# Kernel tuning notes

Hardware: AMD Instinct MI355X
Metric: run time of the kernel (lower is better)

Reference implementation:

```python
import jax, jax.numpy as jnp
import numpy as np

EMB = 768
B, LD, LW, LH = 2, 8, 8, 8        # LR grid = number of windows per axis
HD, HW, HH = 32, 32, 32           # HR volume
LN_EPS = 1e-5


def setup_inputs() -> dict:
    key = jax.random.key(0)
    ks = jax.random.split(key, 12)
    s = 1.0 / np.sqrt(EMB)
    inp = {
        "LR_image": jax.random.normal(ks[0], (B, LD, LW, LH, EMB), jnp.float32),
        "HR_image": jax.random.normal(ks[1], (B, HD, HW, HH, EMB), jnp.float32),
        "Wq_w": jax.random.uniform(ks[2], (EMB, EMB), jnp.float32, -s, s),
        "Wq_b": jax.random.uniform(ks[3], (EMB,), jnp.float32, -s, s),
        "Wk_w": jax.random.uniform(ks[4], (EMB, EMB), jnp.float32, -s, s),
        "Wk_b": jax.random.uniform(ks[5], (EMB,), jnp.float32, -s, s),
        "Wv_w": jax.random.uniform(ks[6], (EMB, EMB), jnp.float32, -s, s),
        "Wv_b": jax.random.uniform(ks[7], (EMB,), jnp.float32, -s, s),
        "Wo_w": jax.random.uniform(ks[8], (EMB, EMB), jnp.float32, -s, s),
        "Wo_b": jax.random.uniform(ks[9], (EMB,), jnp.float32, -s, s),
        "ln_g": jnp.ones((EMB,), jnp.float32),
        "ln_b": jnp.zeros((EMB,), jnp.float32),
        "S_d": 4, "S_w": 4, "S_h": 4,
    }
    return inp


def _window_partition(x, S_d, S_w, S_h):
    # x: [B, D, W, H, C] -> [B, N_blocks, S_d*S_w*S_h, C]
    b, d, w, h, c = x.shape
    x = x.reshape(b, d // S_d, S_d, w // S_w, S_w, h // S_h, S_h, c)
    x = jnp.transpose(x, (0, 2, 4, 6, 1, 3, 5, 7))  # [B,Sd,Sw,Sh,Db,Wb,Hb,C]
    x = x.reshape(b, S_d * S_w * S_h, -1, c)
    return jnp.transpose(x, (0, 2, 1, 3))  # [B, N_blocks, S, C]


def reference(LR_image, HR_image, Wq_w, Wq_b, Wk_w, Wk_b, Wv_w, Wv_b,
              Wo_w, Wo_b, ln_g, ln_b, S_d, S_w, S_h):
    b = LR_image.shape[0]
    c = LR_image.shape[-1]
    # queries: [B, N, 1, C]
    q_in = LR_image.reshape(b, -1, c)[:, :, None, :]
    # windowed keys/values: [B, N, S, C]
    hr = _window_partition(HR_image, S_d, S_w, S_h)
    q = q_in @ Wq_w.T + Wq_b
    k = hr @ Wk_w.T + Wk_b
    v = hr @ Wv_w.T + Wv_b
    scale = 1.0 / jnp.sqrt(jnp.asarray(c, q.dtype))
    scores = jnp.einsum('bnqc,bnsc->bnqs', q, k) * scale  # [B,N,1,S]
    attn = jax.nn.softmax(scores, axis=-1)
    x = jnp.einsum('bnqs,bnsc->bnqc', attn, v).reshape(b, -1, c)
    x = x @ Wo_w.T + Wo_b
    res = q.reshape(b, -1, c) + x  # residual with projected queries
    mu = jnp.mean(res, axis=-1, keepdims=True)
    var = jnp.var(res, axis=-1, keepdims=True)
    return (res - mu) / jnp.sqrt(var + LN_EPS) * ln_g + ln_b
```

## Files before the change

### kernel.cpp

```cpp
#include <hip/hip_runtime.h>
#include <hip/hip_bf16.h>
#include <math.h>

#define EMB 768
#define NB 2
#define NWIN 512
#define NROWS (NB*NWIN)
#define SWIN 64
#define HRDIM 32
#define ROWF (NROWS*EMB)
#define WELEM (EMB*EMB)

using bfrag = __attribute__((ext_vector_type(8))) short;
using f32x4 = __attribute__((ext_vector_type(4))) float;

#define GL16(g, l)  __builtin_amdgcn_global_load_lds(                         \
    (const __attribute__((address_space(1))) void*)(g),                       \
    (__attribute__((address_space(3))) void*)(l), 16, 0, 0)

__global__ __launch_bounds__(256)
void f2b_kernel(const float* __restrict__ in, __hip_bfloat16* __restrict__ out,
                int n8) {
  int i = blockIdx.x * 256 + threadIdx.x;
  if (i >= n8) return;
  float4 a = *(const float4*)&in[(size_t)i * 8];
  float4 b = *(const float4*)&in[(size_t)i * 8 + 4];
  __hip_bfloat16 t[8];
  t[0] = __float2bfloat16(a.x); t[1] = __float2bfloat16(a.y);
  t[2] = __float2bfloat16(a.z); t[3] = __float2bfloat16(a.w);
  t[4] = __float2bfloat16(b.x); t[5] = __float2bfloat16(b.y);
  t[6] = __float2bfloat16(b.z); t[7] = __float2bfloat16(b.w);
  *(uint4*)&out[(size_t)i * 8] = *(const uint4*)t;
}

__global__ __launch_bounds__(256)
void f2b3_kernel(const float* __restrict__ inA, __hip_bfloat16* __restrict__ outA,
                 const float* __restrict__ inB, __hip_bfloat16* __restrict__ outB,
                 const float* __restrict__ inC, __hip_bfloat16* __restrict__ outC) {
  const float* in = (blockIdx.y == 0) ? inA : (blockIdx.y == 1) ? inB : inC;
  __hip_bfloat16* out = (blockIdx.y == 0) ? outA : (blockIdx.y == 1) ? outB : outC;
  int i = blockIdx.x * 256 + threadIdx.x;
  float4 a = *(const float4*)&in[(size_t)i * 8];
  float4 b = *(const float4*)&in[(size_t)i * 8 + 4];
  __hip_bfloat16 t[8];
  t[0] = __float2bfloat16(a.x); t[1] = __float2bfloat16(a.y);
  t[2] = __float2bfloat16(a.z); t[3] = __float2bfloat16(a.w);
  t[4] = __float2bfloat16(b.x); t[5] = __float2bfloat16(b.y);
  t[6] = __float2bfloat16(b.z); t[7] = __float2bfloat16(b.w);
  *(uint4*)&out[(size_t)i * 8] = *(const uint4*)t;
}

__global__ __launch_bounds__(256)
void f2bT_kernel(const float* __restrict__ in, __hip_bfloat16* __restrict__ out) {
  __shared__ float tile[32][33];
  const int bi = blockIdx.x, bj = blockIdx.y;
  const int c = threadIdx.x & 31, r8 = threadIdx.x >> 5;
#pragma unroll
  for (int rr = 0; rr < 4; ++rr) {
    int r = r8 + rr * 8;
    tile[c][r] = in[(size_t)(bi * 32 + r) * EMB + bj * 32 + c];
  }
  __syncthreads();
#pragma unroll
  for (int rr = 0; rr < 4; ++rr) {
    int n = r8 + rr * 8;
    out[(size_t)(bj * 32 + n) * EMB + bi * 32 + c] = __float2bfloat16(tile[n][c]);
  }
}

template<bool BIAS, bool WF32, bool WB16>
__global__ __launch_bounds__(256)
void gemm_bf16(const __hip_bfloat16* __restrict__ A,
               const __hip_bfloat16* __restrict__ Bm,
               const float* __restrict__ bias,
               float* __restrict__ Cf, __hip_bfloat16* __restrict__ Cb,
               int M, int N) {
  constexpr int K = EMB;
  constexpr int NT = K / 64;
  __shared__ short lsA[3][64 * 64];
  __shared__ short lsB[3][64 * 64];
  const int t = threadIdx.x;
  const int w = t >> 6, lane = t & 63;
  const int lr = lane & 15, lk = lane >> 4;
  const int m0 = blockIdx.y * 64, n0 = blockIdx.x * 64;

  const int r0 = t >> 3, c0 = t & 7;
  const int kc = c0 ^ (r0 & 7);
  const __hip_bfloat16* aptr0 = A + (size_t)(m0 + r0) * K + kc * 8;
  const __hip_bfloat16* aptr1 = A + (size_t)(m0 + r0 + 32) * K + kc * 8;
  const __hip_bfloat16* bptr0 = Bm + (size_t)(n0 + r0) * K + kc * 8;
  const __hip_bfloat16* bptr1 = Bm + (size_t)(n0 + r0 + 32) * K + kc * 8;
  const int wbase = w * 512;

  const int arow = w * 16 + lr;
  int aoff[2], boff[4][2];
#pragma unroll
  for (int ks = 0; ks < 2; ++ks)
    aoff[ks] = arow * 64 + (((ks << 2) | lk) ^ (arow & 7)) * 8;
#pragma unroll
  for (int f = 0; f < 4; ++f) {
    int br = f * 16 + lr;
#pragma unroll
    for (int ks = 0; ks < 2; ++ks)
      boff[f][ks] = br * 64 + (((ks << 2) | lk) ^ (br & 7)) * 8;
  }

  f32x4 acc[4];
#pragma unroll
  for (int f = 0; f < 4; ++f) acc[f] = (f32x4){0.f, 0.f, 0.f, 0.f};

#pragma unroll
  for (int p = 0; p < 2; ++p) {
    int ko = p * 64;
    GL16(aptr0 + ko, &lsA[p][wbase]);
    GL16(aptr1 + ko, &lsA[p][wbase + 2048]);
    GL16(bptr0 + ko, &lsB[p][wbase]);
    GL16(bptr1 + ko, &lsB[p][wbase + 2048]);
  }

#pragma unroll
  for (int kt = 0; kt < NT; ++kt) {
    if (kt + 2 < NT) {
      constexpr int s3[NT + 2] = {0,1,2,0,1,2,0,1,2,0,1,2,0,1};
      const int sl = s3[kt + 2];
      int ko = (kt + 2) * 64;
      GL16(aptr0 + ko, &lsA[sl][wbase]);
      GL16(aptr1 + ko, &lsA[sl][wbase + 2048]);
      GL16(bptr0 + ko, &lsB[sl][wbase]);
      GL16(bptr1 + ko, &lsB[sl][wbase + 2048]);
    }
    if (kt + 2 < NT)      asm volatile("s_waitcnt vmcnt(8)" ::: "memory");
    else if (kt + 1 < NT) asm volatile("s_waitcnt vmcnt(4)" ::: "memory");
    else                  asm volatile("s_waitcnt vmcnt(0)" ::: "memory");
    __builtin_amdgcn_sched_barrier(0);
    __builtin_amdgcn_s_barrier();

    const int cur = kt % 3;
    bfrag a0 = *(const bfrag*)&lsA[cur][aoff[0]];
    bfrag a1 = *(const bfrag*)&lsA[cur][aoff[1]];
    bfrag b00 = *(const bfrag*)&lsB[cur][boff[0][0]];
    bfrag b01 = *(const bfrag*)&lsB[cur][boff[0][1]];
    bfrag b10 = *(const bfrag*)&lsB[cur][boff[1][0]];
    bfrag b11 = *(const bfrag*)&lsB[cur][boff[1][1]];
    bfrag b20 = *(const bfrag*)&lsB[cur][boff[2][0]];
    bfrag b21 = *(const bfrag*)&lsB[cur][boff[2][1]];
    bfrag b30 = *(const bfrag*)&lsB[cur][boff[3][0]];
    bfrag b31 = *(const bfrag*)&lsB[cur][boff[3][1]];
    acc[0] = __builtin_amdgcn_mfma_f32_16x16x32_bf16(a0, b00, acc[0], 0, 0, 0);
    acc[0] = __builtin_amdgcn_mfma_f32_16x16x32_bf16(a1, b01, acc[0], 0, 0, 0);
    acc[1] = __builtin_amdgcn_mfma_f32_16x16x32_bf16(a0, b10, acc[1], 0, 0, 0);
    acc[1] = __builtin_amdgcn_mfma_f32_16x16x32_bf16(a1, b11, acc[1], 0, 0, 0);
    acc[2] = __builtin_amdgcn_mfma_f32_16x16x32_bf16(a0, b20, acc[2], 0, 0, 0);
    acc[2] = __builtin_amdgcn_mfma_f32_16x16x32_bf16(a1, b21, acc[2], 0, 0, 0);
    acc[3] = __builtin_amdgcn_mfma_f32_16x16x32_bf16(a0, b30, acc[3], 0, 0, 0);
    acc[3] = __builtin_amdgcn_mfma_f32_16x16x32_bf16(a1, b31, acc[3], 0, 0, 0);

    asm volatile("s_waitcnt lgkmcnt(0)" ::: "memory");
    __builtin_amdgcn_s_barrier();
    __builtin_amdgcn_sched_barrier(0);
  }

  float bs[4] = {0.f, 0.f, 0.f, 0.f};
  if (BIAS) {
#pragma unroll
    for (int f = 0; f < 4; ++f) bs[f] = bias[n0 + f * 16 + lr];
  }
#pragma unroll
  for (int f = 0; f < 4; ++f) {
    int n = n0 + f * 16 + lr;
#pragma unroll
    for (int j = 0; j < 4; ++j) {
      int m = m0 + w * 16 + lk * 4 + j;
      float v = acc[f][j] + bs[f];
      if (WF32) Cf[(size_t)m * N + n] = v;
      if (WB16) Cb[(size_t)m * N + n] = __float2bfloat16(v);
    }
  }
}

__global__ __launch_bounds__(512)
void attn_kernel(const float* __restrict__ HR, const float* __restrict__ qt,
                 __hip_bfloat16* __restrict__ zb) {
  const int g = blockIdx.x;
  const int b = g >> 9;
  const int n = g & 511;
  const int db = n >> 6, wb = (n >> 3) & 7, hb = n & 7;

  __shared__ float qs[EMB];
  __shared__ float sc[SWIN];
  __shared__ int   vb[SWIN];
  __shared__ short win[SWIN][EMB];

  const int t = threadIdx.x;
  const int w = t >> 6, lane = t & 63;

  if (t < 192)
    *(float4*)&qs[t * 4] = *(const float4*)&qt[(size_t)g * EMB + t * 4];
  if (t < SWIN) {
    int sd = t >> 4, sw = (t >> 2) & 3, sh = t & 3;
    int D = db * 4 + sd, W = wb * 4 + sw, H = hb * 4 + sh;
    vb[t] = (((b * HRDIM + D) * HRDIM + W) * HRDIM + H) * EMB;
  }
  __syncthreads();

  float4 qv[3];
#pragma unroll
  for (int r = 0; r < 3; ++r)
    qv[r] = *(const float4*)&qs[(lane + r * 64) * 4];

  float4 hv[8][3];
#pragma unroll
  for (int i = 0; i < 8; ++i) {
    const float* row = HR + vb[w * 8 + i];
#pragma unroll
    for (int r = 0; r < 3; ++r)
      hv[i][r] = *(const float4*)&row[(lane + r * 64) * 4];
  }

  float p[8];
#pragma unroll
  for (int i = 0; i < 8; ++i) {
    float acc = 0.f;
#pragma unroll
    for (int r = 0; r < 3; ++r) {
      acc = fmaf(hv[i][r].x, qv[r].x, acc);
      acc = fmaf(hv[i][r].y, qv[r].y, acc);
      acc = fmaf(hv[i][r].z, qv[r].z, acc);
      acc = fmaf(hv[i][r].w, qv[r].w, acc);
      __hip_bfloat16 o[4];
      o[0] = __float2bfloat16(hv[i][r].x);
      o[1] = __float2bfloat16(hv[i][r].y);
      o[2] = __float2bfloat16(hv[i][r].z);
      o[3] = __float2bfloat16(hv[i][r].w);
      *(uint2*)&win[w * 8 + i][(lane + r * 64) * 4] = *(const uint2*)o;
    }
    p[i] = acc;
  }
#pragma unroll
  for (int i = 0; i < 8; ++i) {
#pragma unroll
    for (int o = 32; o > 0; o >>= 1) p[i] += __shfl_xor(p[i], o, 64);
    if (lane == 0) sc[w * 8 + i] = p[i];
  }
  __syncthreads();

  if (w == 0) {
    const float scale = 0.036084391824351615f;
    float v = sc[lane] * scale;
    float mx = v;
#pragma unroll
    for (int o = 32; o > 0; o >>= 1) mx = fmaxf(mx, __shfl_xor(mx, o, 64));
    float e = expf(v - mx);
    float sum = e;
#pragma unroll
    for (int o = 32; o > 0; o >>= 1) sum += __shfl_xor(sum, o, 64);
    sc[lane] = e / sum;
  }
  __syncthreads();

  if (t < 384) {
    float a0 = 0.f, a1 = 0.f;
#pragma unroll 8
    for (int s = 0; s < SWIN; ++s) {
      float a = sc[s];
      unsigned pk = *(const unsigned*)&win[s][t * 2];
      float h0 = __bfloat162float(*(const __hip_bfloat16*)&pk);
      unsigned hi = pk >> 16;
      float h1 = __bfloat162float(*(const __hip_bfloat16*)&hi);
      a0 = fmaf(a, h0, a0);
      a1 = fmaf(a, h1, a1);
    }
    __hip_bfloat16 o[2];
    o[0] = __float2bfloat16(a0);
    o[1] = __float2bfloat16(a1);
    *(unsigned*)&zb[(size_t)g * EMB + t * 2] = *(const unsigned*)o;
  }
}

__global__ __launch_bounds__(256)
void resid_ln_kernel(const float* __restrict__ Q, const float* __restrict__ X,
                     const float* __restrict__ gma, const float* __restrict__ bta,
                     float* __restrict__ out) {
  const int row = blockIdx.x;
  const int t = threadIdx.x;
  const int wave = t >> 6, lane = t & 63;
  __shared__ float red[4];

  float v[3];
  float s = 0.f;
#pragma unroll
  for (int r = 0; r < 3; ++r) {
    int c = t + r * 256;
    v[r] = Q[(size_t)row * EMB + c] + X[(size_t)row * EMB + c];
    s += v[r];
  }
#pragma unroll
  for (int o = 32; o > 0; o >>= 1) s += __shfl_xor(s, o, 64);
  if (lane == 0) red[wave] = s;
  __syncthreads();
  float mu = (red[0] + red[1] + red[2] + red[3]) * (1.f / EMB);
  __syncthreads();

  float q = 0.f;
#pragma unroll
  for (int r = 0; r < 3; ++r) {
    float d = v[r] - mu;
    q += d * d;
  }
#pragma unroll
  for (int o = 32; o > 0; o >>= 1) q += __shfl_xor(q, o, 64);
  if (lane == 0) red[wave] = q;
  __syncthreads();
  float var = (red[0] + red[1] + red[2] + red[3]) * (1.f / EMB);
  float inv = rsqrtf(var + 1e-5f);

#pragma unroll
  for (int r = 0; r < 3; ++r) {
    int c = t + r * 256;
    out[(size_t)row * EMB + c] = (v[r] - mu) * inv * gma[c] + bta[c];
  }
}

extern "C" void kernel_launch(void* const* d_in, const int* in_sizes, int n_in,
                              void* d_out, int out_size, void* d_ws, size_t ws_size,
                              hipStream_t stream) {
  const float* LR  = (const float*)d_in[0];
  const float* HR  = (const float*)d_in[1];
  const float* Wq  = (const float*)d_in[2];
  const float* bq  = (const float*)d_in[3];
  const float* Wk  = (const float*)d_in[4];
  const float* Wv  = (const float*)d_in[6];
  const float* bv  = (const float*)d_in[7];
  const float* Wo  = (const float*)d_in[8];
  const float* bo  = (const float*)d_in[9];
  const float* lng = (const float*)d_in[10];
  const float* lnb = (const float*)d_in[11];
  float* out = (float*)d_out;

  char* ws = (char*)d_ws;
  float* Qf = (float*)(ws + 0);
  float* qt = (float*)(ws + 3145728);
  float* x  = (float*)(ws + 6291456);
  __hip_bfloat16* LRb  = (__hip_bfloat16*)(ws + 9437184);
  __hip_bfloat16* Qb   = (__hip_bfloat16*)(ws + 11010048);
  __hip_bfloat16* zb   = (__hip_bfloat16*)(ws + 12582912);
  __hip_bfloat16* yb   = (__hip_bfloat16*)(ws + 14155776);
  __hip_bfloat16* Wqb  = (__hip_bfloat16*)(ws + 15728640);
  __hip_bfloat16* WkTb = (__hip_bfloat16*)(ws + 16908288);
  __hip_bfloat16* Wvb  = (__hip_bfloat16*)(ws + 18087936);
  __hip_bfloat16* Wob  = (__hip_bfloat16*)(ws + 19267584);

  dim3 blk(256);
  dim3 gg(EMB / 64, NROWS / 64);

  f2b_kernel<<<dim3(ROWF / 8 / 256), blk, 0, stream>>>(LR, LRb, ROWF / 8);
  f2b3_kernel<<<dim3(WELEM / 8 / 256, 3), blk, 0, stream>>>(
      Wq, Wqb, Wv, Wvb, Wo, Wob);
  f2bT_kernel<<<dim3(24, 24), blk, 0, stream>>>(Wk, WkTb);

  gemm_bf16<true, true, true><<<gg, blk, 0, stream>>>(
      LRb, Wqb, bq, Qf, Qb, NROWS, EMB);
  gemm_bf16<false, true, false><<<gg, blk, 0, stream>>>(
      Qb, WkTb, nullptr, qt, nullptr, NROWS, EMB);
  attn_kernel<<<dim3(NROWS), dim3(512), 0, stream>>>(HR, qt, zb);
  gemm_bf16<true, false, true><<<gg, blk, 0, stream>>>(
      zb, Wvb, bv, nullptr, yb, NROWS, EMB);
  gemm_bf16<true, true, false><<<gg, blk, 0, stream>>>(
      yb, Wob, bo, x, nullptr, NROWS, EMB);
  resid_ln_kernel<<<dim3(NROWS), blk, 0, stream>>>(Qf, x, lng, lnb, out);
}
```

Before: 92.21 us.

## Precompose weight products and use online-softmax attention with fused conversions

Weight products Wq·Wk and Wo·Wv are precomputed per call with a batched bf16 GEMM, and the matching biases are folded by a small bias kernel. The query projection and the q·Wk projection then run as a single batched GEMM from the LR input, and the V and O projections collapse into one GEMM. The attention kernel becomes a register-resident online softmax with per-wave partials merged through shared memory, dropping the bf16 window copy in LDS. This removes two activation-sized GEMMs and several launches, at the cost of two weight-sized GEMMs per call and extra rounding from the bf16 composed weights.

```diff
diff --git a/kernel.cpp b/kernel.cpp
--- a/kernel.cpp
+++ b/kernel.cpp
@@ -19,8 +19,13 @@
     (__attribute__((address_space(3))) void*)(l), 16, 0, 0)
 
 __global__ __launch_bounds__(256)
-void f2b_kernel(const float* __restrict__ in, __hip_bfloat16* __restrict__ out,
-                int n8) {
+void f2b3_kernel(const float* __restrict__ iA, __hip_bfloat16* __restrict__ oA, int nA,
+                 const float* __restrict__ iB, __hip_bfloat16* __restrict__ oB, int nB,
+                 const float* __restrict__ iC, __hip_bfloat16* __restrict__ oC, int nC) {
+  const float* in; __hip_bfloat16* out; int n8;
+  if (blockIdx.y == 0)      { in = iA; out = oA; n8 = nA; }
+  else if (blockIdx.y == 1) { in = iB; out = oB; n8 = nB; }
+  else                      { in = iC; out = oC; n8 = nC; }
   int i = blockIdx.x * 256 + threadIdx.x;
   if (i >= n8) return;
   float4 a = *(const float4*)&in[(size_t)i * 8];
@@ -34,24 +39,13 @@
 }
 
 __global__ __launch_bounds__(256)
-void f2b3_kernel(const float* __restrict__ inA, __hip_bfloat16* __restrict__ outA,
-                 const float* __restrict__ inB, __hip_bfloat16* __restrict__ outB,
-                 const float* __restrict__ inC, __hip_bfloat16* __restrict__ outC) {
-  const float* in = (blockIdx.y == 0) ? inA : (blockIdx.y == 1) ? inB : inC;
-  __hip_bfloat16* out = (blockIdx.y == 0) ? outA : (blockIdx.y == 1) ? outB : outC;
-  int i = blockIdx.x * 256 + threadIdx.x;
-  float4 a = *(const float4*)&in[(size_t)i * 8];
-  float4 b = *(const float4*)&in[(size_t)i * 8 + 4];
-  __hip_bfloat16 t[8];
-  t[0] = __float2bfloat16(a.x); t[1] = __float2bfloat16(a.y);
-  t[2] = __float2bfloat16(a.z); t[3] = __float2bfloat16(a.w);
-  t[4] = __float2bfloat16(b.x); t[5] = __float2bfloat16(b.y);
-  t[6] = __float2bfloat16(b.z); t[7] = __float2bfloat16(b.w);
-  *(uint4*)&out[(size_t)i * 8] = *(const uint4*)t;
-}
-
-__global__ __launch_bounds__(256)
-void f2bT_kernel(const float* __restrict__ in, __hip_bfloat16* __restrict__ out) {
+void f2bT3_kernel(const float* __restrict__ iA, __hip_bfloat16* __restrict__ oA,
+                  const float* __restrict__ iB, __hip_bfloat16* __restrict__ oB,
+                  const float* __restrict__ iC, __hip_bfloat16* __restrict__ oC) {
+  const float* in; __hip_bfloat16* out;
+  if (blockIdx.z == 0)      { in = iA; out = oA; }
+  else if (blockIdx.z == 1) { in = iB; out = oB; }
+  else                      { in = iC; out = oC; }
   __shared__ float tile[32][33];
   const int bi = blockIdx.x, bj = blockIdx.y;
   const int c = threadIdx.x & 31, r8 = threadIdx.x >> 5;
@@ -68,15 +62,45 @@
   }
 }
 
+__global__ __launch_bounds__(256)
+void bias_kernel(const float* __restrict__ bq, const float* __restrict__ Wk,
+                 const float* __restrict__ Wo, const float* __restrict__ bv,
+                 const float* __restrict__ bo, float* __restrict__ bqk,
+                 float* __restrict__ bvo) {
+  int i = blockIdx.x * 256 + threadIdx.x;
+  if (i < EMB) {
+    float s = 0.f;
+#pragma unroll 4
+    for (int c = 0; c < EMB; ++c) s = fmaf(bq[c], Wk[(size_t)c * EMB + i], s);
+    bqk[i] = s;
+  } else {
+    int p = i - EMB;
+    float s = bo[p];
+#pragma unroll 4
+    for (int n = 0; n < EMB; ++n) s = fmaf(Wo[(size_t)p * EMB + n], bv[n], s);
+    bvo[p] = s;
+  }
+}
+
 template<bool BIAS, bool WF32, bool WB16>
 __global__ __launch_bounds__(256)
-void gemm_bf16(const __hip_bfloat16* __restrict__ A,
-               const __hip_bfloat16* __restrict__ Bm,
-               const float* __restrict__ bias,
-               float* __restrict__ Cf, __hip_bfloat16* __restrict__ Cb,
-               int M, int N) {
+void gemm_bf16(const __hip_bfloat16* __restrict__ A0,
+               const __hip_bfloat16* __restrict__ A1,
+               const __hip_bfloat16* __restrict__ B0,
+               const __hip_bfloat16* __restrict__ B1,
+               const float* __restrict__ bias0, const float* __restrict__ bias1,
+               float* __restrict__ Cf0, float* __restrict__ Cf1,
+               __hip_bfloat16* __restrict__ Cb0, __hip_bfloat16* __restrict__ Cb1,
+               int N) {
   constexpr int K = EMB;
   constexpr int NT = K / 64;
+  const int zi = blockIdx.z;
+  const __hip_bfloat16* A  = zi ? A1 : A0;
+  const __hip_bfloat16* Bm = zi ? B1 : B0;
+  const float* bias = zi ? bias1 : bias0;
+  float* Cf = zi ? Cf1 : Cf0;
+  __hip_bfloat16* Cb = zi ? Cb1 : Cb0;
+
   __shared__ short lsA[3][64 * 64];
   __shared__ short lsB[3][64 * 64];
   const int t = threadIdx.x;
@@ -186,93 +210,88 @@
   const int n = g & 511;
   const int db = n >> 6, wb = (n >> 3) & 7, hb = n & 7;
 
-  __shared__ float qs[EMB];
-  __shared__ float sc[SWIN];
-  __shared__ int   vb[SWIN];
-  __shared__ short win[SWIN][EMB];
+  __shared__ float zp[8][EMB];
+  __shared__ float ml[8][2];
 
   const int t = threadIdx.x;
   const int w = t >> 6, lane = t & 63;
 
-  if (t < 192)
-    *(float4*)&qs[t * 4] = *(const float4*)&qt[(size_t)g * EMB + t * 4];
-  if (t < SWIN) {
-    int sd = t >> 4, sw = (t >> 2) & 3, sh = t & 3;
-    int D = db * 4 + sd, W = wb * 4 + sw, H = hb * 4 + sh;
-    vb[t] = (((b * HRDIM + D) * HRDIM + W) * HRDIM + H) * EMB;
-  }
-  __syncthreads();
-
   float4 qv[3];
 #pragma unroll
   for (int r = 0; r < 3; ++r)
-    qv[r] = *(const float4*)&qs[(lane + r * 64) * 4];
-
-  float4 hv[8][3];
+    qv[r] = *(const float4*)&qt[(size_t)g * EMB + (lane + r * 64) * 4];
+
+  const float* rows[8];
 #pragma unroll
   for (int i = 0; i < 8; ++i) {
-    const float* row = HR + vb[w * 8 + i];
-#pragma unroll
-    for (int r = 0; r < 3; ++r)
-      hv[i][r] = *(const float4*)&row[(lane + r * 64) * 4];
-  }
-
-  float p[8];
+    int s = w * 8 + i;
+    int D = db * 4 + (s >> 4), W = wb * 4 + ((s >> 2) & 3), H = hb * 4 + (s & 3);
+    rows[i] = HR + (size_t)((((b * HRDIM + D) * HRDIM + W) * HRDIM + H)) * EMB;
+  }
+
+  const float scale = 0.036084391824351615f;
+  float m = -3.0e38f, l = 0.f;
+  float4 z0 = {0,0,0,0}, z1 = {0,0,0,0}, z2 = {0,0,0,0};
+
+  float4 h0 = *(const float4*)&rows[0][lane * 4];
+  float4 h1 = *(const float4*)&rows[0][(lane + 64) * 4];
+  float4 h2 = *(const float4*)&rows[0][(lane + 128) * 4];
+
 #pragma unroll
   for (int i = 0; i < 8; ++i) {
-    float acc = 0.f;
-#pragma unroll
-    for (int r = 0; r < 3; ++r) {
-      acc = fmaf(hv[i][r].x, qv[r].x, acc);
-      acc = fmaf(hv[i][r].y, qv[r].y, acc);
-      acc = fmaf(hv[i][r].z, qv[r].z, acc);
-      acc = fmaf(hv[i][r].w, qv[r].w, acc);
-      __hip_bfloat16 o[4];
-      o[0] = __float2bfloat16(hv[i][r].x);
-      o[1] = __float2bfloat16(hv[i][r].y);
-      o[2] = __float2bfloat16(hv[i][r].z);
-      o[3] = __float2bfloat16(hv[i][r].w);
-      *(uint2*)&win[w * 8 + i][(lane + r * 64) * 4] = *(const uint2*)o;
+    float4 n0, n1, n2;
+    if (i < 7) {
+      n0 = *(const float4*)&rows[i + 1][lane * 4];
+      n1 = *(const float4*)&rows[i + 1][(lane + 64) * 4];
+      n2 = *(const float4*)&rows[i + 1][(lane + 128) * 4];
     }
-    p[i] = acc;
-  }
-#pragma unroll
-  for (int i = 0; i < 8; ++i) {
-#pragma unroll
-    for (int o = 32; o > 0; o >>= 1) p[i] += __shfl_xor(p[i], o, 64);
-    if (lane == 0) sc[w * 8 + i] = p[i];
-  }
-  __syncthreads();
-
-  if (w == 0) {
-    const float scale = 0.036084391824351615f;
-    float v = sc[lane] * scale;
-    float mx = v;
-#pragma unroll
-    for (int o = 32; o > 0; o >>= 1) mx = fmaxf(mx, __shfl_xor(mx, o, 64));
-    float e = expf(v - mx);
-    float sum = e;
-#pragma unroll
-    for (int o = 32; o > 0; o >>= 1) sum += __shfl_xor(sum, o, 64);
-    sc[lane] = e / sum;
-  }
+    float p = 0.f;
+    p = fmaf(h0.x, qv[0].x, p); p = fmaf(h0.y, qv[0].y, p);
+    p = fmaf(h0.z, qv[0].z, p); p = fmaf(h0.w, qv[0].w, p);
+    p = fmaf(h1.x, qv[1].x, p); p = fmaf(h1.y, qv[1].y, p);
+    p = fmaf(h1.z, qv[1].z, p); p = fmaf(h1.w, qv[1].w, p);
+    p = fmaf(h2.x, qv[2].x, p); p = fmaf(h2.y, qv[2].y, p);
+    p = fmaf(h2.z, qv[2].z, p); p = fmaf(h2.w, qv[2].w, p);
+#pragma unroll
+    for (int o = 32; o > 0; o >>= 1) p += __shfl_xor(p, o, 64);
+    p *= scale;
+    float mn = fmaxf(m, p);
+    float f = expf(m - mn);
+    float e = expf(p - mn);
+    z0.x = fmaf(e, h0.x, z0.x * f); z0.y = fmaf(e, h0.y, z0.y * f);
+    z0.z = fmaf(e, h0.z, z0.z * f); z0.w = fmaf(e, h0.w, z0.w * f);
+    z1.x = fmaf(e, h1.x, z1.x * f); z1.y = fmaf(e, h1.y, z1.y * f);
+    z1.z = fmaf(e, h1.z, z1.z * f); z1.w = fmaf(e, h1.w, z1.w * f);
+    z2.x = fmaf(e, h2.x, z2.x * f); z2.y = fmaf(e, h2.y, z2.y * f);
+    z2.z = fmaf(e, h2.z, z2.z * f); z2.w = fmaf(e, h2.w, z2.w * f);
+    l = fmaf(l, f, e);
+    m = mn;
+    if (i < 7) { h0 = n0; h1 = n1; h2 = n2; }
+  }
+
+  *(float4*)&zp[w][lane * 4] = z0;
+  *(float4*)&zp[w][(lane + 64) * 4] = z1;
+  *(float4*)&zp[w][(lane + 128) * 4] = z2;
+  if (lane == 0) { ml[w][0] = m; ml[w][1] = l; }
   __syncthreads();
 
   if (t < 384) {
-    float a0 = 0.f, a1 = 0.f;
-#pragma unroll 8
-    for (int s = 0; s < SWIN; ++s) {
-      float a = sc[s];
-      unsigned pk = *(const unsigned*)&win[s][t * 2];
-      float h0 = __bfloat162float(*(const __hip_bfloat16*)&pk);
-      unsigned hi = pk >> 16;
-      float h1 = __bfloat162float(*(const __hip_bfloat16*)&hi);
-      a0 = fmaf(a, h0, a0);
-      a1 = fmaf(a, h1, a1);
+    float M = -3.0e38f;
+#pragma unroll
+    for (int w8 = 0; w8 < 8; ++w8) M = fmaxf(M, ml[w8][0]);
+    float L = 0.f, a0 = 0.f, a1 = 0.f;
+#pragma unroll
+    for (int w8 = 0; w8 < 8; ++w8) {
+      float ew = expf(ml[w8][0] - M);
+      L = fmaf(ml[w8][1], ew, L);
+      float2 v = *(const float2*)&zp[w8][t * 2];
+      a0 = fmaf(v.x, ew, a0);
+      a1 = fmaf(v.y, ew, a1);
     }
+    float rl = 1.f / L;
     __hip_bfloat16 o[2];
-    o[0] = __float2bfloat16(a0);
-    o[1] = __float2bfloat16(a1);
+    o[0] = __float2bfloat16(a0 * rl);
+    o[1] = __float2bfloat16(a1 * rl);
     *(unsigned*)&zb[(size_t)g * EMB + t * 2] = *(const unsigned*)o;
   }
 }
@@ -341,31 +360,32 @@
   float* Qf = (float*)(ws + 0);
   float* qt = (float*)(ws + 3145728);
   float* x  = (float*)(ws + 6291456);
-  __hip_bfloat16* LRb  = (__hip_bfloat16*)(ws + 9437184);
-  __hip_bfloat16* Qb   = (__hip_bfloat16*)(ws + 11010048);
-  __hip_bfloat16* zb   = (__hip_bfloat16*)(ws + 12582912);
-  __hip_bfloat16* yb   = (__hip_bfloat16*)(ws + 14155776);
-  __hip_bfloat16* Wqb  = (__hip_bfloat16*)(ws + 15728640);
-  __hip_bfloat16* WkTb = (__hip_bfloat16*)(ws + 16908288);
-  __hip_bfloat16* Wvb  = (__hip_bfloat16*)(ws + 18087936);
-  __hip_bfloat16* Wob  = (__hip_bfloat16*)(ws + 19267584);
+  __hip_bfloat16* LRb  = (__hip_bfloat16*)(ws +  9437184);
+  __hip_bfloat16* zb   = (__hip_bfloat16*)(ws + 11010048);
+  __hip_bfloat16* Wqb  = (__hip_bfloat16*)(ws + 12582912);
+  __hip_bfloat16* Wob  = (__hip_bfloat16*)(ws + 13762560);
+  __hip_bfloat16* WqTb = (__hip_bfloat16*)(ws + 14942208);
+  __hip_bfloat16* WkTb = (__hip_bfloat16*)(ws + 16121856);
+  __hip_bfloat16* WvTb = (__hip_bfloat16*)(ws + 17301504);
+  __hip_bfloat16* Wqkb = (__hip_bfloat16*)(ws + 18481152);
+  __hip_bfloat16* Wvob = (__hip_bfloat16*)(ws + 19660800);
+  float* bqk = (float*)(ws + 20840448);
+  float* bvo = (float*)(ws + 20843520);
 
   dim3 blk(256);
-  dim3 gg(EMB / 64, NROWS / 64);
-
-  f2b_kernel<<<dim3(ROWF / 8 / 256), blk, 0, stream>>>(LR, LRb, ROWF / 8);
-  f2b3_kernel<<<dim3(WELEM / 8 / 256, 3), blk, 0, stream>>>(
-      Wq, Wqb, Wv, Wvb, Wo, Wob);
-  f2bT_kernel<<<dim3(24, 24), blk, 0, stream>>>(Wk, WkTb);
-
-  gemm_bf16<true, true, true><<<gg, blk, 0, stream>>>(
-      LRb, Wqb, bq, Qf, Qb, NROWS, EMB);
-  gemm_bf16<false, true, false><<<gg, blk, 0, stream>>>(
-      Qb, WkTb, nullptr, qt, nullptr, NROWS, EMB);
+
+  f2b3_kernel<<<dim3(384, 3), blk, 0, stream>>>(
+      LR, LRb, ROWF / 8, Wq, Wqb, WELEM / 8, Wo, Wob, WELEM / 8);
+  f2bT3_kernel<<<dim3(24, 24, 3), blk, 0, stream>>>(
+      Wq, WqTb, Wk, WkTb, Wv, WvTb);
+  gemm_bf16<false, false, true><<<dim3(12, 12, 2), blk, 0, stream>>>(
+      WkTb, Wob, WqTb, WvTb, nullptr, nullptr,
+      nullptr, nullptr, Wqkb, Wvob, EMB);
+  bias_kernel<<<dim3(6), blk, 0, stream>>>(bq, Wk, Wo, bv, bo, bqk, bvo);
+  gemm_bf16<true, true, false><<<dim3(12, 16, 2), blk, 0, stream>>>(
+      LRb, LRb, Wqb, Wqkb, bq, bqk, Qf, qt, nullptr, nullptr, EMB);
   attn_kernel<<<dim3(NROWS), dim3(512), 0, stream>>>(HR, qt, zb);
-  gemm_bf16<true, false, true><<<gg, blk, 0, stream>>>(
-      zb, Wvb, bv, nullptr, yb, NROWS, EMB);
-  gemm_bf16<true, true, false><<<gg, blk, 0, stream>>>(
-      yb, Wob, bo, x, nullptr, NROWS, EMB);
+  gemm_bf16<true, true, false><<<dim3(12, 16, 1), blk, 0, stream>>>(
+      zb, zb, Wvob, Wvob, bvo, bvo, x, x, nullptr, nullptr, EMB);
   resid_ln_kernel<<<dim3(NROWS), blk, 0, stream>>>(Qf, x, lng, lnb, out);
 }
```

Result: slower. 136.1 us (+47.6%).
